# Performance work log

Measured on AMD Instinct MI355X. Metric: run time of the kernel, lower is better.

## Reference

```python
import jax, jax.numpy as jnp
import numpy as np

NUM_HEAD = 8


def setup_inputs() -> dict:
    key = jax.random.key(0)
    k1, k2, k3, k4 = jax.random.split(key, 4)
    B, C, H, W = 16, 512, 64, 64
    x = jax.random.normal(k1, (B, C, H, W), dtype=jnp.float32)
    w_qkv = jax.random.normal(k2, (3 * C, C), dtype=jnp.float32) * 0.02  # Conv2d 1x1, no bias
    w_proj = jax.random.normal(k3, (C, C), dtype=jnp.float32) * 0.02
    b_proj = jax.random.normal(k4, (C,), dtype=jnp.float32) * 0.02
    return {"x": x, "w_qkv": w_qkv, "w_proj": w_proj, "b_proj": b_proj}


def reference(x, w_qkv, w_proj, b_proj):
    B, C, H, W = x.shape
    nh = NUM_HEAD
    hd = C // nh
    scale = hd ** (-0.5)
    # 1x1 conv == channel matmul
    qkv = jnp.einsum('oc,bchw->bohw', w_qkv, x)  # [B, 3C, H, W]
    q, k, v = jnp.split(qkv, 3, axis=1)
    q = q.reshape(B, nh, hd, H * W)
    k = k.reshape(B, nh, hd, H * W)
    v = v.reshape(B, nh, hd, H * W)
    # NOTE: faithful to source: contracts over the spatial (last) axis,
    # producing a [B, nh, hd, hd] matrix.
    attn = jnp.einsum('bnqd,bnkd->bnqk', q, k) * scale
    attn = jax.nn.softmax(attn, axis=-1)
    # Faithful to source: 'k' and 'v' are both summed independently (outer sum),
    # exactly as torch.einsum computes it.
    out = jnp.einsum('bnqk,bnvd->bnqd', attn, v)
    out = out.reshape(B, C, H, W)
    return jnp.einsum('oc,bchw->bohw', w_proj, out) + b_proj[None, :, None, None]
```

## Files before the change

kernel.cpp:

```cpp
#include <hip/hip_runtime.h>

#define CDIM 512
#define NH 8
#define HWDIM 4096
#define TPOS 64
#define NTILE 4
#define NT 512

__global__ __launch_bounds__(256) void prep_kernel(
    const float* __restrict__ wqkv, const float* __restrict__ wproj,
    float* __restrict__ wvT, float* __restrict__ wp) {
  int idx = blockIdx.x * 256 + threadIdx.x;
  if (idx < 4096) {
    int c = idx >> 3, n = idx & 7;
    const float* p = wqkv + (size_t)(1024 + n * 64) * CDIM + c;
    float s = 0.f;
#pragma unroll 8
    for (int j = 0; j < 64; ++j) s += p[(size_t)j * CDIM];
    wvT[idx] = s;
  } else if (idx < 8192) {
    int i2 = idx - 4096;
    int o = i2 >> 3, n = i2 & 7;
    const float* p = wproj + (size_t)o * CDIM + n * 64;
    float s = 0.f;
#pragma unroll 8
    for (int j = 0; j < 64; ++j) s += p[j];
    wp[i2] = s;
  }
}

__global__ __launch_bounds__(NT, 1) void fused_kernel(
    const float* __restrict__ x, const float* __restrict__ bias,
    const float* __restrict__ wvT, const float* __restrict__ wp,
    float* __restrict__ y) {
  __shared__ __align__(16) float sWv[4096];
  __shared__ __align__(16) float sWp[4096];
  __shared__ __align__(16) float sB[512];
  __shared__ __align__(16) float sS[2][8][NH][TPOS];

  const int t = threadIdx.x;
  for (int i = t; i < 4096; i += NT) { sWv[i] = wvT[i]; sWp[i] = wp[i]; }
  if (t < 512) sB[t] = bias[t];
  __syncthreads();

  const int wave = t >> 6;
  const int lane = t & 63;
  const int pos0 = blockIdx.x * (NTILE * TPOS);
  const int b = pos0 >> 12;
  const int hw0 = pos0 & (HWDIM - 1);
  const float* xb = x + ((size_t)b * CDIM) * HWDIM + hw0 + lane;
  float* yb = y + ((size_t)b * CDIM) * HWDIM + hw0 + lane;

  const int g0 = wave * 64;
  const int rot  = (blockIdx.x * 37) & 63;
  const int rot2 = (blockIdx.x * 23) & 63;

  float S2[NH];
  float acc[NH];

#pragma unroll
  for (int n = 0; n < NH; ++n) acc[n] = 0.f;
#pragma unroll 8
  for (int i = 0; i < 64; ++i) {
    const int c = g0 + ((i + rot) & 63);
    const float xv = xb[(size_t)c * HWDIM];
    const float4 w0 = *(const float4*)&sWv[c * 8];
    const float4 w1 = *(const float4*)&sWv[c * 8 + 4];
    acc[0] = fmaf(w0.x, xv, acc[0]); acc[1] = fmaf(w0.y, xv, acc[1]);
    acc[2] = fmaf(w0.z, xv, acc[2]); acc[3] = fmaf(w0.w, xv, acc[3]);
    acc[4] = fmaf(w1.x, xv, acc[4]); acc[5] = fmaf(w1.y, xv, acc[5]);
    acc[6] = fmaf(w1.z, xv, acc[6]); acc[7] = fmaf(w1.w, xv, acc[7]);
  }
#pragma unroll
  for (int n = 0; n < NH; ++n) sS[0][wave][n][lane] = acc[n];
  __syncthreads();
#pragma unroll
  for (int n = 0; n < NH; ++n) {
    float s = 0.f;
#pragma unroll
    for (int w = 0; w < 8; ++w) s += sS[0][w][n][lane];
    S2[n] = s;
  }

  for (int tt = 1; tt < NTILE; ++tt) {
    const float* xbt = xb + tt * TPOS;
    float* ybp = yb + (tt - 1) * TPOS;
#pragma unroll
    for (int n = 0; n < NH; ++n) acc[n] = 0.f;
#pragma unroll 8
    for (int i = 0; i < 64; ++i) {
      const int o = g0 + ((i + rot2) & 63);
      const float4 p0 = *(const float4*)&sWp[o * 8];
      const float4 p1 = *(const float4*)&sWp[o * 8 + 4];
      float r = sB[o];
      r = fmaf(p0.x, S2[0], r); r = fmaf(p0.y, S2[1], r);
      r = fmaf(p0.z, S2[2], r); r = fmaf(p0.w, S2[3], r);
      r = fmaf(p1.x, S2[4], r); r = fmaf(p1.y, S2[5], r);
      r = fmaf(p1.z, S2[6], r); r = fmaf(p1.w, S2[7], r);
      __builtin_nontemporal_store(r, ybp + (size_t)o * HWDIM);
      const int c = g0 + ((i + rot) & 63);
      const float xv = xbt[(size_t)c * HWDIM];
      const float4 w0 = *(const float4*)&sWv[c * 8];
      const float4 w1 = *(const float4*)&sWv[c * 8 + 4];
      acc[0] = fmaf(w0.x, xv, acc[0]); acc[1] = fmaf(w0.y, xv, acc[1]);
      acc[2] = fmaf(w0.z, xv, acc[2]); acc[3] = fmaf(w0.w, xv, acc[3]);
      acc[4] = fmaf(w1.x, xv, acc[4]); acc[5] = fmaf(w1.y, xv, acc[5]);
      acc[6] = fmaf(w1.z, xv, acc[6]); acc[7] = fmaf(w1.w, xv, acc[7]);
    }
    const int buf = tt & 1;
#pragma unroll
    for (int n = 0; n < NH; ++n) sS[buf][wave][n][lane] = acc[n];
    __syncthreads();
#pragma unroll
    for (int n = 0; n < NH; ++n) {
      float s = 0.f;
#pragma unroll
      for (int w = 0; w < 8; ++w) s += sS[buf][w][n][lane];
      S2[n] = s;
    }
  }

  {
    float* ybp = yb + (NTILE - 1) * TPOS;
#pragma unroll 8
    for (int i = 0; i < 64; ++i) {
      const int o = g0 + ((i + rot2) & 63);
      const float4 p0 = *(const float4*)&sWp[o * 8];
      const float4 p1 = *(const float4*)&sWp[o * 8 + 4];
      float r = sB[o];
      r = fmaf(p0.x, S2[0], r); r = fmaf(p0.y, S2[1], r);
      r = fmaf(p0.z, S2[2], r); r = fmaf(p0.w, S2[3], r);
      r = fmaf(p1.x, S2[4], r); r = fmaf(p1.y, S2[5], r);
      r = fmaf(p1.z, S2[6], r); r = fmaf(p1.w, S2[7], r);
      __builtin_nontemporal_store(r, ybp + (size_t)o * HWDIM);
    }
  }
}

extern "C" void kernel_launch(void* const* d_in, const int* in_sizes, int n_in,
                              void* d_out, int out_size, void* d_ws, size_t ws_size,
                              hipStream_t stream) {
  const float* x     = (const float*)d_in[0];
  const float* wqkv  = (const float*)d_in[1];
  const float* wproj = (const float*)d_in[2];
  const float* bproj = (const float*)d_in[3];
  float* y = (float*)d_out;

  float* wvT = (float*)d_ws;
  float* wp  = wvT + 4096;

  prep_kernel<<<32, 256, 0, stream>>>(wqkv, wproj, wvT, wp);
  fused_kernel<<<(16 * HWDIM) / (NTILE * TPOS), NT, 0, stream>>>(x, bproj, wvT, wp, y);
}
```

Baseline: 260.3 us.

## Specialize waves into reader and writer groups pipelining across tiles

Splits the block's eight waves into four reader waves, which load x and reduce over 128 channels each, and four writer waves, which compute and store the projected output for 128 output channels. The two groups work on adjacent tiles through a double-buffered shared-memory array. Readers now batch 16 strided global loads before their FMAs, to raise memory-level parallelism. The cost is that only half the waves issue loads at any time, and the per-block channel rotation that spread DRAM accesses across blocks is dropped.

```diff
diff --git a/kernel.cpp b/kernel.cpp
--- a/kernel.cpp
+++ b/kernel.cpp
@@ -36,7 +36,7 @@
   __shared__ __align__(16) float sWv[4096];
   __shared__ __align__(16) float sWp[4096];
   __shared__ __align__(16) float sB[512];
-  __shared__ __align__(16) float sS[2][8][NH][TPOS];
+  __shared__ __align__(16) float sS[2][4][NH][TPOS];
 
   const int t = threadIdx.x;
   for (int i = t; i < 4096; i += NT) { sWv[i] = wvT[i]; sWp[i] = wp[i]; }
@@ -51,89 +51,61 @@
   const float* xb = x + ((size_t)b * CDIM) * HWDIM + hw0 + lane;
   float* yb = y + ((size_t)b * CDIM) * HWDIM + hw0 + lane;
 
-  const int g0 = wave * 64;
-  const int rot  = (blockIdx.x * 37) & 63;
-  const int rot2 = (blockIdx.x * 23) & 63;
+  const bool reader = (wave < 4);
+  const int c0 = wave * 128;
+  const int o0 = (wave - 4) * 128;
 
-  float S2[NH];
-  float acc[NH];
-
+  for (int tt = 0; tt <= NTILE; ++tt) {
+    if (reader) {
+      if (tt < NTILE) {
+        const float* xt = xb + tt * TPOS;
+        float acc[NH];
 #pragma unroll
-  for (int n = 0; n < NH; ++n) acc[n] = 0.f;
-#pragma unroll 8
-  for (int i = 0; i < 64; ++i) {
-    const int c = g0 + ((i + rot) & 63);
-    const float xv = xb[(size_t)c * HWDIM];
-    const float4 w0 = *(const float4*)&sWv[c * 8];
-    const float4 w1 = *(const float4*)&sWv[c * 8 + 4];
-    acc[0] = fmaf(w0.x, xv, acc[0]); acc[1] = fmaf(w0.y, xv, acc[1]);
-    acc[2] = fmaf(w0.z, xv, acc[2]); acc[3] = fmaf(w0.w, xv, acc[3]);
-    acc[4] = fmaf(w1.x, xv, acc[4]); acc[5] = fmaf(w1.y, xv, acc[5]);
-    acc[6] = fmaf(w1.z, xv, acc[6]); acc[7] = fmaf(w1.w, xv, acc[7]);
-  }
+        for (int n = 0; n < NH; ++n) acc[n] = 0.f;
+        for (int g = 0; g < 8; ++g) {
+          float xv[16];
 #pragma unroll
-  for (int n = 0; n < NH; ++n) sS[0][wave][n][lane] = acc[n];
-  __syncthreads();
+          for (int j = 0; j < 16; ++j)
+            xv[j] = xt[(size_t)(c0 + g * 16 + j) * HWDIM];
 #pragma unroll
-  for (int n = 0; n < NH; ++n) {
-    float s = 0.f;
+          for (int j = 0; j < 16; ++j) {
+            const int c = c0 + g * 16 + j;
+            const float4 w0 = *(const float4*)&sWv[c * 8];
+            const float4 w1 = *(const float4*)&sWv[c * 8 + 4];
+            acc[0] = fmaf(w0.x, xv[j], acc[0]); acc[1] = fmaf(w0.y, xv[j], acc[1]);
+            acc[2] = fmaf(w0.z, xv[j], acc[2]); acc[3] = fmaf(w0.w, xv[j], acc[3]);
+            acc[4] = fmaf(w1.x, xv[j], acc[4]); acc[5] = fmaf(w1.y, xv[j], acc[5]);
+            acc[6] = fmaf(w1.z, xv[j], acc[6]); acc[7] = fmaf(w1.w, xv[j], acc[7]);
+          }
+        }
+        const int buf = tt & 1;
 #pragma unroll
-    for (int w = 0; w < 8; ++w) s += sS[0][w][n][lane];
-    S2[n] = s;
-  }
-
-  for (int tt = 1; tt < NTILE; ++tt) {
-    const float* xbt = xb + tt * TPOS;
-    float* ybp = yb + (tt - 1) * TPOS;
+        for (int n = 0; n < NH; ++n) sS[buf][wave][n][lane] = acc[n];
+      }
+    } else {
+      if (tt >= 1) {
+        const int p = (tt - 1) & 1;
+        float S2[NH];
 #pragma unroll
-    for (int n = 0; n < NH; ++n) acc[n] = 0.f;
-#pragma unroll 8
-    for (int i = 0; i < 64; ++i) {
-      const int o = g0 + ((i + rot2) & 63);
-      const float4 p0 = *(const float4*)&sWp[o * 8];
-      const float4 p1 = *(const float4*)&sWp[o * 8 + 4];
-      float r = sB[o];
-      r = fmaf(p0.x, S2[0], r); r = fmaf(p0.y, S2[1], r);
-      r = fmaf(p0.z, S2[2], r); r = fmaf(p0.w, S2[3], r);
-      r = fmaf(p1.x, S2[4], r); r = fmaf(p1.y, S2[5], r);
-      r = fmaf(p1.z, S2[6], r); r = fmaf(p1.w, S2[7], r);
-      __builtin_nontemporal_store(r, ybp + (size_t)o * HWDIM);
-      const int c = g0 + ((i + rot) & 63);
-      const float xv = xbt[(size_t)c * HWDIM];
-      const float4 w0 = *(const float4*)&sWv[c * 8];
-      const float4 w1 = *(const float4*)&sWv[c * 8 + 4];
-      acc[0] = fmaf(w0.x, xv, acc[0]); acc[1] = fmaf(w0.y, xv, acc[1]);
-      acc[2] = fmaf(w0.z, xv, acc[2]); acc[3] = fmaf(w0.w, xv, acc[3]);
-      acc[4] = fmaf(w1.x, xv, acc[4]); acc[5] = fmaf(w1.y, xv, acc[5]);
-      acc[6] = fmaf(w1.z, xv, acc[6]); acc[7] = fmaf(w1.w, xv, acc[7]);
+        for (int n = 0; n < NH; ++n)
+          S2[n] = sS[p][0][n][lane] + sS[p][1][n][lane] +
+                  sS[p][2][n][lane] + sS[p][3][n][lane];
+        float* yt = yb + (tt - 1) * TPOS;
+#pragma unroll 4
+        for (int oo = 0; oo < 128; ++oo) {
+          const int o = o0 + oo;
+          const float4 p0 = *(const float4*)&sWp[o * 8];
+          const float4 p1 = *(const float4*)&sWp[o * 8 + 4];
+          float r = sB[o];
+          r = fmaf(p0.x, S2[0], r); r = fmaf(p0.y, S2[1], r);
+          r = fmaf(p0.z, S2[2], r); r = fmaf(p0.w, S2[3], r);
+          r = fmaf(p1.x, S2[4], r); r = fmaf(p1.y, S2[5], r);
+          r = fmaf(p1.z, S2[6], r); r = fmaf(p1.w, S2[7], r);
+          __builtin_nontemporal_store(r, yt + (size_t)o * HWDIM);
+        }
+      }
     }
-    const int buf = tt & 1;
-#pragma unroll
-    for (int n = 0; n < NH; ++n) sS[buf][wave][n][lane] = acc[n];
     __syncthreads();
-#pragma unroll
-    for (int n = 0; n < NH; ++n) {
-      float s = 0.f;
-#pragma unroll
-      for (int w = 0; w < 8; ++w) s += sS[buf][w][n][lane];
-      S2[n] = s;
-    }
-  }
-
-  {
-    float* ybp = yb + (NTILE - 1) * TPOS;
-#pragma unroll 8
-    for (int i = 0; i < 64; ++i) {
-      const int o = g0 + ((i + rot2) & 63);
-      const float4 p0 = *(const float4*)&sWp[o * 8];
-      const float4 p1 = *(const float4*)&sWp[o * 8 + 4];
-      float r = sB[o];
-      r = fmaf(p0.x, S2[0], r); r = fmaf(p0.y, S2[1], r);
-      r = fmaf(p0.z, S2[2], r); r = fmaf(p0.w, S2[3], r);
-      r = fmaf(p1.x, S2[4], r); r = fmaf(p1.y, S2[5], r);
-      r = fmaf(p1.z, S2[6], r); r = fmaf(p1.w, S2[7], r);
-      __builtin_nontemporal_store(r, ybp + (size_t)o * HWDIM);
-    }
   }
 }
 
```

Result: slower. 275.6 us (+5.9%).
